# Kernel optimization log

Measured on AMD Instinct MI355X. Metric: run time of the kernel, lower is better.

## Reference

```python
import jax, jax.numpy as jnp
import numpy as np

SEQ, BATCH, IN, HID = 512, 64, 512, 1024

def setup_inputs() -> dict:
    key = jax.random.key(0)
    ks = jax.random.split(key, 7)
    s = 1.0 / np.sqrt(IN + HID)
    return {
        "embedding": jax.random.normal(ks[0], (SEQ, BATCH, IN), dtype=jnp.float32),
        "init_h": jnp.zeros((BATCH, HID), dtype=jnp.float32),
        "Wz": jax.random.uniform(ks[1], (IN + HID, HID), minval=-s, maxval=s, dtype=jnp.float32),
        "bz": jax.random.uniform(ks[2], (HID,), minval=-s, maxval=s, dtype=jnp.float32),
        "Wr": jax.random.uniform(ks[3], (IN + HID, HID), minval=-s, maxval=s, dtype=jnp.float32),
        "br": jax.random.uniform(ks[4], (HID,), minval=-s, maxval=s, dtype=jnp.float32),
        "Wm": jax.random.uniform(ks[5], (IN + HID, HID), minval=-s, maxval=s, dtype=jnp.float32),
        "bm": jax.random.uniform(ks[6], (HID,), minval=-s, maxval=s, dtype=jnp.float32),
    }

def reference(embedding, init_h, Wz, bz, Wr, br, Wm, bm):
    # Split gate weights into input/hidden parts so per-step work is two GEMVs
    # on [B,IN] and [B,HID] rather than a concat (same math as Linear on concat).
    Wz_x, Wz_h = Wz[:IN], Wz[IN:]
    Wr_x, Wr_h = Wr[:IN], Wr[IN:]
    Wm_x, Wm_h = Wm[:IN], Wm[IN:]
    # Precompute input projections for all timesteps (parallel GEMMs).
    xz = jnp.einsum('sbi,ih->sbh', embedding, Wz_x) + bz  # [S,B,H]
    xr = jnp.einsum('sbi,ih->sbh', embedding, Wr_x) + br
    xm = jnp.einsum('sbi,ih->sbh', embedding, Wm_x) + bm

    def step(h, xs):
        xz_t, xr_t, xm_t = xs
        z = jax.nn.sigmoid(xz_t + h @ Wz_h)
        r = jax.nn.sigmoid(xr_t + h @ Wr_h)
        h_tilde = jnp.tanh(xm_t + (r * h) @ Wm_h)
        h_new = (1.0 - z) * h + z * h_tilde
        return h_new, h_new

    _, hs = jax.lax.scan(step, init_h, (xz, xr, xm))  # hs: [S,B,H]
    # torch.stack(hidden_states, dim=1) -> [B, S, H]
    return jnp.transpose(hs, (1, 0, 2))
```

## Files before the change

kernel.cpp:

```cpp
#include <hip/hip_runtime.h>
#include <cstdint>
#include <cstddef>

#define SEQ   512
#define BATCH 64
#define INDIM 512
#define HID   1024

typedef short bf16x8 __attribute__((ext_vector_type(8)));
typedef float f32x4  __attribute__((ext_vector_type(4)));
typedef unsigned long long ull;
typedef unsigned int u32;

#define MFMA16(A,B,C) __builtin_amdgcn_mfma_f32_16x16x32_bf16(A,B,C,0,0,0)

#define WS_FH  0
#define WS_FR  16384
#define WS_HP  32768
#define WS_RP  (WS_HP + 524288)
#define WS_WHI (WS_RP + 262144)
#define WS_WLO (WS_WHI + 9437184)
#define WS_END (WS_WLO + 9437184)

__device__ __forceinline__ unsigned short f2bf(float f) {
  unsigned u = __float_as_uint(f);
  unsigned r = (u + 0x7fffu + ((u >> 16) & 1u)) >> 16;
  return (unsigned short)r;
}
__device__ __forceinline__ float bf2f(unsigned short h) {
  return __uint_as_float(((unsigned)h) << 16);
}
__device__ __forceinline__ void splitf(float x, unsigned short& hi, unsigned short& lo) {
  unsigned short h = f2bf(x);
  float r = x - bf2f(h);
  hi = h; lo = f2bf(r);
}

__global__ void prep_w(const float* __restrict__ Wz, const float* __restrict__ Wr,
                       const float* __restrict__ Wm,
                       bf16x8* __restrict__ wh, bf16x8* __restrict__ wl) {
  int n    = blockIdx.x * 256 + threadIdx.x;
  int lane = n & 63;
  int m    = n >> 6;
  int g    = m % 3;
  int m2   = m / 3;
  int kc   = m2 % 48;
  int jb   = m2 / 48;
  const float* W = (g == 0) ? Wz : (g == 1) ? Wr : Wm;
  int k0 = kc*32 + ((lane >> 4) << 3);
  int nn = jb*16 + (lane & 15);
  bf16x8 vh, vl;
  #pragma unroll
  for (int j = 0; j < 8; ++j) {
    unsigned short a, b;
    splitf(W[(size_t)(k0 + j)*HID + nn], a, b);
    vh[j] = (short)a; vl[j] = (short)b;
  }
  wh[n] = vh; wl[n] = vl;
}

__global__ void prep_h(const float* __restrict__ h0, u32* __restrict__ hp) {
  int n = blockIdx.x * 256 + threadIdx.x;
  int b = n >> 7;
  int j = (n & 127) << 3;
  const float* s = h0 + (size_t)b*HID + j;
  float4 f0 = ((const float4*)s)[0];
  float4 f1 = ((const float4*)s)[1];
  float v[8] = {f0.x,f0.y,f0.z,f0.w,f1.x,f1.y,f1.z,f1.w};
  int g     = b >> 4;
  int kc2   = j >> 5;
  int lane2 = (b & 15) + (((j >> 3) & 3) << 4);
  size_t base = (size_t)g*32768 + (size_t)kc2*512 + (size_t)lane2;
  #pragma unroll
  for (int q = 0; q < 8; ++q) {
    unsigned short a, c;
    splitf(v[q], a, c);
    hp[base + (size_t)q*64] = ((u32)a << 16) | (u32)c;
  }
}

__device__ __forceinline__ void waitf(const u32* f, unsigned tgt) {
  for (;;) {
    unsigned v = __hip_atomic_load(f, __ATOMIC_RELAXED, __HIP_MEMORY_SCOPE_AGENT);
    if (__ballot(v >= tgt) == ~0ull) return;
    __builtin_amdgcn_s_sleep(1);
  }
}

__device__ __forceinline__ void loadfrags(bf16x8* Fh, bf16x8* Fl,
                                          const u32* __restrict__ base32) {
  #pragma unroll
  for (int i = 0; i < 8; ++i) {
    u32 wv[8];
    #pragma unroll
    for (int e = 0; e < 8; ++e)
      wv[e] = __hip_atomic_load(base32 + (size_t)i*512 + (size_t)e*64,
                                __ATOMIC_RELAXED, __HIP_MEMORY_SCOPE_AGENT);
    bf16x8 h8, l8;
    #pragma unroll
    for (int e = 0; e < 8; ++e) {
      h8[e] = (short)(wv[e] >> 16);
      l8[e] = (short)(wv[e] & 0xffffu);
    }
    Fh[i] = h8; Fl[i] = l8;
  }
}

__global__ __launch_bounds__(256, 1)
void gru_main(const float* __restrict__ emb,
              const float* __restrict__ bz, const float* __restrict__ br,
              const float* __restrict__ bm, const float* __restrict__ init_h,
              float* __restrict__ out,
              const bf16x8* __restrict__ wh_all, const bf16x8* __restrict__ wl_all,
              u32* __restrict__ hp, u32* __restrict__ rp,
              u32* __restrict__ fh, u32* __restrict__ fr)
{
  const int tid  = threadIdx.x;
  const int w    = tid >> 6;
  const int lane = tid & 63;
  const int jb   = blockIdx.x & 63;
  const int g    = blockIdx.x >> 6;
  const int c    = lane & 15;
  const int q    = lane >> 4;
  const int jc   = jb*16 + c;
  const int rb   = q << 2;
  const int bb   = g*16 + rb;

  u32* fh_g = fh + g*1024;
  u32* fr_g = fr + g*1024;
  const u32* fh_w = fh_g + ((w*16 + c) << 4);
  const u32* fr_w = fr_g + ((w*16 + c) << 4);

  const float bzj = bz[jc], brj = br[jc], bmj = bm[jc];
  float st[4];
  #pragma unroll
  for (int r = 0; r < 4; ++r) st[r] = init_h[(size_t)(bb + r)*HID + jc];

  __shared__ f32x4  red1[3][4][64];
  __shared__ f32x4  red2[4][64];
  __shared__ bf16x8 ewS[96][64];

  for (int i = tid; i < 6144; i += 256) {
    int l = i & 63, row = i >> 6;
    int hl = row / 48, rr2 = row % 48;
    const bf16x8* src = (hl ? wl_all : wh_all) + ((size_t)jb*144 + rr2)*64 + l;
    ewS[row][l] = *src;
  }

  const bf16x8* whB = wh_all + ((size_t)jb*144)*64 + lane;
  const bf16x8* wlB = wl_all + ((size_t)jb*144)*64 + lane;
  bf16x8 Wh[8][3], Wl[8][3];
  #pragma unroll
  for (int i = 0; i < 8; ++i) {
    int kc = 16 + w*8 + i;
    #pragma unroll
    for (int gt = 0; gt < 3; ++gt) {
      Wh[i][gt] = whB[(size_t)(kc*3 + gt)*64];
      Wl[i][gt] = wlB[(size_t)(kc*3 + gt)*64];
    }
  }
  __syncthreads();

  const int kc2w   = jc >> 5;
  const int l2base = ((jc & 31) >> 3) << 4;
  const int e7     = jc & 7;
  const size_t pub_base = (size_t)kc2w*512 + (size_t)e7*64 + (size_t)(l2base + rb);

  const u32* hgrp0 = hp + (size_t)g*32768;
  const u32* hgrp1 = hgrp0 + 16384;
  const u32* rgrp  = rp + (size_t)g*16384;
  const size_t woff = (size_t)w*4096 + (size_t)lane;

  const float* ebase = emb + (size_t)(g*16 + c)*INDIM + (q << 3);

  for (int t = 0; t < SEQ; ++t) {
    f32x4 az  = {0.f,0.f,0.f,0.f};
    f32x4 ar  = {0.f,0.f,0.f,0.f};
    f32x4 amx = {0.f,0.f,0.f,0.f};
    f32x4 amh = {0.f,0.f,0.f,0.f};

    const float* et = ebase + (size_t)t*(BATCH*INDIM);
    #pragma unroll
    for (int qq = 0; qq < 4; ++qq) {
      int kce = w*4 + qq;
      const float* s = et + kce*32;
      float4 f0 = ((const float4*)s)[0];
      float4 f1 = ((const float4*)s)[1];
      float v[8] = {f0.x,f0.y,f0.z,f0.w,f1.x,f1.y,f1.z,f1.w};
      bf16x8 eh, el;
      #pragma unroll
      for (int j = 0; j < 8; ++j) {
        unsigned short a, b;
        splitf(v[j], a, b);
        eh[j] = (short)a; el[j] = (short)b;
      }
      int rowz = kce*3;
      bf16x8 wzh = ewS[rowz+0][lane], wzl = ewS[48+rowz+0][lane];
      bf16x8 wrh = ewS[rowz+1][lane], wrl = ewS[48+rowz+1][lane];
      bf16x8 wmh = ewS[rowz+2][lane], wml = ewS[48+rowz+2][lane];
      az  = MFMA16(eh, wzh, az);  az  = MFMA16(eh, wzl, az);  az  = MFMA16(el, wzh, az);
      ar  = MFMA16(eh, wrh, ar);  ar  = MFMA16(eh, wrl, ar);  ar  = MFMA16(el, wrh, ar);
      amx = MFMA16(eh, wmh, amx); amx = MFMA16(eh, wml, amx); amx = MFMA16(el, wmh, amx);
    }

    const int buf = t & 1;
    if (t > 0) waitf(fh_w, (unsigned)t);
    bf16x8 Ah[8], Al[8];
    loadfrags(Ah, Al, (buf ? hgrp1 : hgrp0) + woff);
    #pragma unroll
    for (int i = 0; i < 8; ++i) {
      az = MFMA16(Ah[i], Wh[i][0], az);
      az = MFMA16(Ah[i], Wl[i][0], az);
      az = MFMA16(Al[i], Wh[i][0], az);
      ar = MFMA16(Ah[i], Wh[i][1], ar);
      ar = MFMA16(Ah[i], Wl[i][1], ar);
      ar = MFMA16(Al[i], Wh[i][1], ar);
    }

    red1[0][w][lane] = az;
    red1[1][w][lane] = ar;
    red1[2][w][lane] = amx;
    __syncthreads();
    f32x4 azF  = red1[0][0][lane] + red1[0][1][lane] + red1[0][2][lane] + red1[0][3][lane];
    f32x4 arF  = red1[1][0][lane] + red1[1][1][lane] + red1[1][2][lane] + red1[1][3][lane];
    f32x4 amxF = red1[2][0][lane] + red1[2][1][lane] + red1[2][2][lane] + red1[2][3][lane];

    if (w == 0) {
      u32 wd[4];
      #pragma unroll
      for (int r = 0; r < 4; ++r) {
        float rr  = 1.f / (1.f + __expf(-(arF[r] + brj)));
        float rhv = rr * st[r];
        unsigned short sh, sl;
        splitf(rhv, sh, sl);
        wd[r] = ((u32)sh << 16) | (u32)sl;
      }
      ull* dst = (ull*)(rp + (size_t)g*16384 + pub_base);
      __hip_atomic_store(dst + 0, (ull)wd[0] | ((ull)wd[1] << 32),
                         __ATOMIC_RELAXED, __HIP_MEMORY_SCOPE_AGENT);
      __hip_atomic_store(dst + 1, (ull)wd[2] | ((ull)wd[3] << 32),
                         __ATOMIC_RELAXED, __HIP_MEMORY_SCOPE_AGENT);
    }
    if (tid == 0) {
      asm volatile("s_waitcnt vmcnt(0)" ::: "memory");
      __hip_atomic_store(fr_g + (jb << 4), (unsigned)(t + 1),
                         __ATOMIC_RELAXED, __HIP_MEMORY_SCOPE_AGENT);
    }

    waitf(fr_w, (unsigned)(t + 1));
    bf16x8 Bh[8], Bl[8];
    loadfrags(Bh, Bl, rgrp + woff);
    float z[4];
    #pragma unroll
    for (int r = 0; r < 4; ++r)
      z[r] = 1.f / (1.f + __expf(-(azF[r] + bzj)));
    #pragma unroll
    for (int i = 0; i < 8; ++i) {
      amh = MFMA16(Bh[i], Wh[i][2], amh);
      amh = MFMA16(Bh[i], Wl[i][2], amh);
      amh = MFMA16(Bl[i], Wh[i][2], amh);
    }

    red2[w][lane] = amh;
    __syncthreads();
    f32x4 amhF = red2[0][lane] + red2[1][lane] + red2[2][lane] + red2[3][lane];

    const int obuf = buf ^ 1;
    float hnv[4];
    u32 hd[4];
    #pragma unroll
    for (int r = 0; r < 4; ++r) {
      float pm = amxF[r] + bmj + amhF[r];
      float e2 = __expf(2.f*pm);
      float htl = 1.f - 2.f/(e2 + 1.f);
      float hn = st[r] + z[r]*(htl - st[r]);
      st[r] = hn; hnv[r] = hn;
      unsigned short sh, sl;
      splitf(hn, sh, sl);
      hd[r] = ((u32)sh << 16) | (u32)sl;
    }
    if (w == 0) {
      ull* hdst = (ull*)(hp + (size_t)g*32768 + (size_t)obuf*16384 + pub_base);
      __hip_atomic_store(hdst + 0, (ull)hd[0] | ((ull)hd[1] << 32),
                         __ATOMIC_RELAXED, __HIP_MEMORY_SCOPE_AGENT);
      __hip_atomic_store(hdst + 1, (ull)hd[2] | ((ull)hd[3] << 32),
                         __ATOMIC_RELAXED, __HIP_MEMORY_SCOPE_AGENT);
    }
    if (tid == 0) {
      asm volatile("s_waitcnt vmcnt(0)" ::: "memory");
      __hip_atomic_store(fh_g + (jb << 4), (unsigned)(t + 1),
                         __ATOMIC_RELAXED, __HIP_MEMORY_SCOPE_AGENT);
    }

    if (w == 1) {
      #pragma unroll
      for (int r = 0; r < 4; ++r)
        __builtin_nontemporal_store(hnv[r],
            out + (size_t)(bb + r)*(SEQ*HID) + (size_t)t*HID + jc);
    }
  }
}

extern "C" void kernel_launch(void* const* d_in, const int* in_sizes, int n_in,
                              void* d_out, int out_size, void* d_ws, size_t ws_size,
                              hipStream_t stream) {
  const float* emb = (const float*)d_in[0];
  const float* h0  = (const float*)d_in[1];
  const float* Wz  = (const float*)d_in[2];
  const float* bz  = (const float*)d_in[3];
  const float* Wr  = (const float*)d_in[4];
  const float* br  = (const float*)d_in[5];
  const float* Wm  = (const float*)d_in[6];
  const float* bm  = (const float*)d_in[7];
  float* out = (float*)d_out;

  if (ws_size < (size_t)WS_END) return;

  char* ws = (char*)d_ws;
  u32*    fhp = (u32*)(ws + WS_FH);
  u32*    frp = (u32*)(ws + WS_FR);
  u32*    hpp = (u32*)(ws + WS_HP);
  u32*    rpp = (u32*)(ws + WS_RP);
  bf16x8* wph = (bf16x8*)(ws + WS_WHI);
  bf16x8* wpl = (bf16x8*)(ws + WS_WLO);

  hipMemsetAsync(ws, 0, 32768, stream);
  prep_w<<<2304, 256, 0, stream>>>(Wz, Wr, Wm, wph, wpl);
  prep_h<<<32,   256, 0, stream>>>(h0, hpp);
  gru_main<<<256, 256, 0, stream>>>(emb, bz, br, bm, h0, out,
                                    wph, wpl, hpp, rpp, fhp, frp);
}
```

Baseline: 4.508 ms.

## Split GRU block work across eight waves with register-resident input weights

Doubles the threads per block from 4 to 8 waves, so each wave handles half the K-chunks of the hidden and input GEMVs, and the partial sums are reduced across eight waves in shared memory. The input-projection weights now stay in registers instead of LDS. The embedding for the next timestep is prefetched. The m-gate input MFMAs are moved after the r publish so they overlap the wait. Flag polling is limited to 8 lanes per wave to reduce atomic traffic. The cost is a larger shared-memory reduction and more waves contending per CU.

```diff
diff --git a/kernel.cpp b/kernel.cpp
--- a/kernel.cpp
+++ b/kernel.cpp
@@ -79,18 +79,20 @@
   }
 }
 
-__device__ __forceinline__ void waitf(const u32* f, unsigned tgt) {
+__device__ __forceinline__ void waitf(const u32* f, unsigned tgt, bool poller) {
   for (;;) {
-    unsigned v = __hip_atomic_load(f, __ATOMIC_RELAXED, __HIP_MEMORY_SCOPE_AGENT);
+    unsigned v = tgt;
+    if (poller)
+      v = __hip_atomic_load(f, __ATOMIC_RELAXED, __HIP_MEMORY_SCOPE_AGENT);
     if (__ballot(v >= tgt) == ~0ull) return;
     __builtin_amdgcn_s_sleep(1);
   }
 }
 
-__device__ __forceinline__ void loadfrags(bf16x8* Fh, bf16x8* Fl,
-                                          const u32* __restrict__ base32) {
-  #pragma unroll
-  for (int i = 0; i < 8; ++i) {
+__device__ __forceinline__ void loadfrags4(bf16x8* Fh, bf16x8* Fl,
+                                           const u32* __restrict__ base32) {
+  #pragma unroll
+  for (int i = 0; i < 4; ++i) {
     u32 wv[8];
     #pragma unroll
     for (int e = 0; e < 8; ++e)
@@ -106,7 +108,10 @@
   }
 }
 
-__global__ __launch_bounds__(256, 1)
+#define SUM8(A, l) (((A[0][l]+A[1][l])+(A[2][l]+A[3][l])) + \
+                    ((A[4][l]+A[5][l])+(A[6][l]+A[7][l])))
+
+__global__ __launch_bounds__(512, 1)
 void gru_main(const float* __restrict__ emb,
               const float* __restrict__ bz, const float* __restrict__ br,
               const float* __restrict__ bm, const float* __restrict__ init_h,
@@ -128,38 +133,40 @@
 
   u32* fh_g = fh + g*1024;
   u32* fr_g = fr + g*1024;
-  const u32* fh_w = fh_g + ((w*16 + c) << 4);
-  const u32* fr_w = fr_g + ((w*16 + c) << 4);
+  const u32* fh_w = fh_g + ((w*8 + (lane & 7)) << 4);
+  const u32* fr_w = fr_g + ((w*8 + (lane & 7)) << 4);
+  const bool poller = (lane < 8);
 
   const float bzj = bz[jc], brj = br[jc], bmj = bm[jc];
   float st[4];
   #pragma unroll
   for (int r = 0; r < 4; ++r) st[r] = init_h[(size_t)(bb + r)*HID + jc];
 
-  __shared__ f32x4  red1[3][4][64];
-  __shared__ f32x4  red2[4][64];
-  __shared__ bf16x8 ewS[96][64];
-
-  for (int i = tid; i < 6144; i += 256) {
-    int l = i & 63, row = i >> 6;
-    int hl = row / 48, rr2 = row % 48;
-    const bf16x8* src = (hl ? wl_all : wh_all) + ((size_t)jb*144 + rr2)*64 + l;
-    ewS[row][l] = *src;
-  }
+  __shared__ f32x4 redA[2][8][64];
+  __shared__ f32x4 redM[2][8][64];
 
   const bf16x8* whB = wh_all + ((size_t)jb*144)*64 + lane;
   const bf16x8* wlB = wl_all + ((size_t)jb*144)*64 + lane;
-  bf16x8 Wh[8][3], Wl[8][3];
-  #pragma unroll
-  for (int i = 0; i < 8; ++i) {
-    int kc = 16 + w*8 + i;
+  bf16x8 Wh[4][3], Wl[4][3];
+  #pragma unroll
+  for (int i = 0; i < 4; ++i) {
+    int kc = 16 + w*4 + i;
     #pragma unroll
     for (int gt = 0; gt < 3; ++gt) {
       Wh[i][gt] = whB[(size_t)(kc*3 + gt)*64];
       Wl[i][gt] = wlB[(size_t)(kc*3 + gt)*64];
     }
   }
-  __syncthreads();
+  bf16x8 Eh[2][3], El[2][3];
+  #pragma unroll
+  for (int j = 0; j < 2; ++j) {
+    int kce = w*2 + j;
+    #pragma unroll
+    for (int gt = 0; gt < 3; ++gt) {
+      Eh[j][gt] = whB[(size_t)(kce*3 + gt)*64];
+      El[j][gt] = wlB[(size_t)(kce*3 + gt)*64];
+    }
+  }
 
   const int kc2w   = jc >> 5;
   const int l2base = ((jc & 31) >> 3) << 4;
@@ -169,61 +176,67 @@
   const u32* hgrp0 = hp + (size_t)g*32768;
   const u32* hgrp1 = hgrp0 + 16384;
   const u32* rgrp  = rp + (size_t)g*16384;
-  const size_t woff = (size_t)w*4096 + (size_t)lane;
+  const size_t woff = (size_t)w*2048 + (size_t)lane;
 
   const float* ebase = emb + (size_t)(g*16 + c)*INDIM + (q << 3);
 
+  float4 pf[2][2];
+  #pragma unroll
+  for (int j = 0; j < 2; ++j) {
+    const float* s = ebase + (size_t)(w*2 + j)*32;
+    pf[j][0] = ((const float4*)s)[0];
+    pf[j][1] = ((const float4*)s)[1];
+  }
+
   for (int t = 0; t < SEQ; ++t) {
-    f32x4 az  = {0.f,0.f,0.f,0.f};
-    f32x4 ar  = {0.f,0.f,0.f,0.f};
-    f32x4 amx = {0.f,0.f,0.f,0.f};
-    f32x4 amh = {0.f,0.f,0.f,0.f};
-
-    const float* et = ebase + (size_t)t*(BATCH*INDIM);
-    #pragma unroll
-    for (int qq = 0; qq < 4; ++qq) {
-      int kce = w*4 + qq;
-      const float* s = et + kce*32;
-      float4 f0 = ((const float4*)s)[0];
-      float4 f1 = ((const float4*)s)[1];
-      float v[8] = {f0.x,f0.y,f0.z,f0.w,f1.x,f1.y,f1.z,f1.w};
-      bf16x8 eh, el;
-      #pragma unroll
-      for (int j = 0; j < 8; ++j) {
+    bf16x8 eh[2], el[2];
+    #pragma unroll
+    for (int j = 0; j < 2; ++j) {
+      float v[8] = {pf[j][0].x, pf[j][0].y, pf[j][0].z, pf[j][0].w,
+                    pf[j][1].x, pf[j][1].y, pf[j][1].z, pf[j][1].w};
+      bf16x8 a8, b8;
+      #pragma unroll
+      for (int k = 0; k < 8; ++k) {
         unsigned short a, b;
-        splitf(v[j], a, b);
-        eh[j] = (short)a; el[j] = (short)b;
-      }
-      int rowz = kce*3;
-      bf16x8 wzh = ewS[rowz+0][lane], wzl = ewS[48+rowz+0][lane];
-      bf16x8 wrh = ewS[rowz+1][lane], wrl = ewS[48+rowz+1][lane];
-      bf16x8 wmh = ewS[rowz+2][lane], wml = ewS[48+rowz+2][lane];
-      az  = MFMA16(eh, wzh, az);  az  = MFMA16(eh, wzl, az);  az  = MFMA16(el, wzh, az);
-      ar  = MFMA16(eh, wrh, ar);  ar  = MFMA16(eh, wrl, ar);  ar  = MFMA16(el, wrh, ar);
-      amx = MFMA16(eh, wmh, amx); amx = MFMA16(eh, wml, amx); amx = MFMA16(el, wmh, amx);
+        splitf(v[k], a, b);
+        a8[k] = (short)a; b8[k] = (short)b;
+      }
+      eh[j] = a8; el[j] = b8;
+    }
+
+    f32x4 az = {0.f,0.f,0.f,0.f};
+    f32x4 ar = {0.f,0.f,0.f,0.f};
+
+    #pragma unroll
+    for (int j = 0; j < 2; ++j) {
+      az = MFMA16(eh[j], Eh[j][0], az);
+      az = MFMA16(eh[j], El[j][0], az);
+      az = MFMA16(el[j], Eh[j][0], az);
+      ar = MFMA16(eh[j], Eh[j][1], ar);
+      ar = MFMA16(eh[j], El[j][1], ar);
+      ar = MFMA16(el[j], Eh[j][1], ar);
     }
 
     const int buf = t & 1;
-    if (t > 0) waitf(fh_w, (unsigned)t);
-    bf16x8 Ah[8], Al[8];
-    loadfrags(Ah, Al, (buf ? hgrp1 : hgrp0) + woff);
-    #pragma unroll
-    for (int i = 0; i < 8; ++i) {
-      az = MFMA16(Ah[i], Wh[i][0], az);
-      az = MFMA16(Ah[i], Wl[i][0], az);
-      az = MFMA16(Al[i], Wh[i][0], az);
-      ar = MFMA16(Ah[i], Wh[i][1], ar);
-      ar = MFMA16(Ah[i], Wl[i][1], ar);
-      ar = MFMA16(Al[i], Wh[i][1], ar);
-    }
-
-    red1[0][w][lane] = az;
-    red1[1][w][lane] = ar;
-    red1[2][w][lane] = amx;
+    if (t > 0) waitf(fh_w, (unsigned)t, poller);
+    {
+      bf16x8 Ah[4], Al[4];
+      loadfrags4(Ah, Al, (buf ? hgrp1 : hgrp0) + woff);
+      #pragma unroll
+      for (int i = 0; i < 4; ++i) {
+        az = MFMA16(Ah[i], Wh[i][0], az);
+        az = MFMA16(Ah[i], Wl[i][0], az);
+        az = MFMA16(Al[i], Wh[i][0], az);
+        ar = MFMA16(Ah[i], Wh[i][1], ar);
+        ar = MFMA16(Ah[i], Wl[i][1], ar);
+        ar = MFMA16(Al[i], Wh[i][1], ar);
+      }
+    }
+
+    redA[0][w][lane] = az;
+    redA[1][w][lane] = ar;
     __syncthreads();
-    f32x4 azF  = red1[0][0][lane] + red1[0][1][lane] + red1[0][2][lane] + red1[0][3][lane];
-    f32x4 arF  = red1[1][0][lane] + red1[1][1][lane] + red1[1][2][lane] + red1[1][3][lane];
-    f32x4 amxF = red1[2][0][lane] + red1[2][1][lane] + red1[2][2][lane] + red1[2][3][lane];
+    f32x4 arF = SUM8(redA[1], lane);
 
     if (w == 0) {
       u32 wd[4];
@@ -247,23 +260,47 @@
                          __ATOMIC_RELAXED, __HIP_MEMORY_SCOPE_AGENT);
     }
 
-    waitf(fr_w, (unsigned)(t + 1));
-    bf16x8 Bh[8], Bl[8];
-    loadfrags(Bh, Bl, rgrp + woff);
+    f32x4 amx = {0.f,0.f,0.f,0.f};
+    #pragma unroll
+    for (int j = 0; j < 2; ++j) {
+      amx = MFMA16(eh[j], Eh[j][2], amx);
+      amx = MFMA16(eh[j], El[j][2], amx);
+      amx = MFMA16(el[j], Eh[j][2], amx);
+    }
+    f32x4 azF = SUM8(redA[0], lane);
     float z[4];
     #pragma unroll
     for (int r = 0; r < 4; ++r)
       z[r] = 1.f / (1.f + __expf(-(azF[r] + bzj)));
-    #pragma unroll
-    for (int i = 0; i < 8; ++i) {
-      amh = MFMA16(Bh[i], Wh[i][2], amh);
-      amh = MFMA16(Bh[i], Wl[i][2], amh);
-      amh = MFMA16(Bl[i], Wh[i][2], amh);
-    }
-
-    red2[w][lane] = amh;
+    {
+      int tn = (t + 1 < SEQ) ? (t + 1) : t;
+      const float* et = ebase + (size_t)tn*(BATCH*INDIM);
+      #pragma unroll
+      for (int j = 0; j < 2; ++j) {
+        const float* s = et + (size_t)(w*2 + j)*32;
+        pf[j][0] = ((const float4*)s)[0];
+        pf[j][1] = ((const float4*)s)[1];
+      }
+    }
+
+    waitf(fr_w, (unsigned)(t + 1), poller);
+    f32x4 amh = {0.f,0.f,0.f,0.f};
+    {
+      bf16x8 Bh[4], Bl[4];
+      loadfrags4(Bh, Bl, rgrp + woff);
+      #pragma unroll
+      for (int i = 0; i < 4; ++i) {
+        amh = MFMA16(Bh[i], Wh[i][2], amh);
+        amh = MFMA16(Bh[i], Wl[i][2], amh);
+        amh = MFMA16(Bl[i], Wh[i][2], amh);
+      }
+    }
+
+    redM[0][w][lane] = amx;
+    redM[1][w][lane] = amh;
     __syncthreads();
-    f32x4 amhF = red2[0][lane] + red2[1][lane] + red2[2][lane] + red2[3][lane];
+    f32x4 amxF = SUM8(redM[0], lane);
+    f32x4 amhF = SUM8(redM[1], lane);
 
     const int obuf = buf ^ 1;
     float hnv[4];
@@ -327,6 +364,6 @@
   hipMemsetAsync(ws, 0, 32768, stream);
   prep_w<<<2304, 256, 0, stream>>>(Wz, Wr, Wm, wph, wpl);
   prep_h<<<32,   256, 0, stream>>>(h0, hpp);
-  gru_main<<<256, 256, 0, stream>>>(emb, bz, br, bm, h0, out,
+  gru_main<<<256, 512, 0, stream>>>(emb, bz, br, bm, h0, out,
                                     wph, wpl, hpp, rpp, fhp, frp);
 }
```

New measurement: 4.499 ms. Within noise of the previous version (-0.2%).
